# Kernel tuning notes

Measured on AMD Instinct MI355X. Metric: run time of the kernel, lower is better.

The kernel has to match this reference:

```python
import jax, jax.numpy as jnp
import numpy as np

BS, T, D_IN, NH, D_OUT = 8, 1024, 64, 8, 1024
DK = 2


def setup_inputs() -> dict:
    key = jax.random.key(0)
    ks = jax.random.split(key, 10)
    X = jax.random.normal(ks[0], (BS, T, D_IN), dtype=jnp.float32)
    # Linear(d_in, 2*Nh) params (torch stores weight as (out, in))
    Wq_w = jax.random.normal(ks[1], (2 * NH, D_IN), dtype=jnp.float32) * (1.0 / np.sqrt(D_IN))
    Wq_b = jax.random.normal(ks[2], (2 * NH,), dtype=jnp.float32) * 0.02
    Wk_w = jax.random.normal(ks[3], (2 * NH, D_IN), dtype=jnp.float32) * (1.0 / np.sqrt(D_IN))
    Wk_b = jax.random.normal(ks[4], (2 * NH,), dtype=jnp.float32) * 0.02
    Wkey_ = jax.random.normal(ks[5], (2, 2), dtype=jnp.float32)
    u = jax.random.normal(ks[6], (T, 2), dtype=jnp.float32)
    # R[t,l] = [(l-t)^2, (l-t)]
    rel = jnp.arange(T)[None, :] - jnp.arange(T)[:, None]  # (T,T)
    R = jnp.stack([rel.astype(jnp.float32) ** 2, rel.astype(jnp.float32)], axis=-1)  # (T,T,2)
    attention_center = jax.random.normal(ks[7], (NH, 1), dtype=jnp.float32) * 2.0
    alpha = jax.random.normal(ks[8], (1,), dtype=jnp.float32)
    W_w = jax.random.normal(ks[9], (D_OUT, T), dtype=jnp.float32) * (1.0 / np.sqrt(T))
    W_b = jnp.zeros((D_OUT,), dtype=jnp.float32)
    return {"X": X, "Wq_w": Wq_w, "Wq_b": Wq_b, "Wk_w": Wk_w, "Wk_b": Wk_b,
            "Wkey_": Wkey_, "u": u, "R": R, "attention_center": attention_center,
            "alpha": alpha, "W_w": W_w, "W_b": W_b}


def reference(X, Wq_w, Wq_b, Wk_w, Wk_b, Wkey_, u, R, attention_center, alpha, W_w, W_b):
    bs, T_, d_in = X.shape
    Nh = attention_center.shape[0]
    query = (X @ Wq_w.T + Wq_b).reshape(bs, T_, Nh, DK)
    key_ = (X @ Wk_w.T + Wk_b).reshape(bs, T_, Nh, DK)
    r_delta = jnp.einsum('de,tle->tld', Wkey_, R)  # (T,T,2)
    v = -alpha * jnp.concatenate([jnp.ones_like(attention_center), -2.0 * attention_center], axis=-1)  # (Nh,2)
    first = jnp.einsum('bthd,blhd->bthl', query, key_)
    second = jnp.einsum('bthd,tld->bthl', query, r_delta)
    third = jnp.einsum('ld,bthd->blht', u, key_)  # added positionally, matching torch
    fourth = jnp.einsum('hd,tld->thl', v, r_delta)
    scores = first + second + third + fourth[None]  # (bs,T,Nh,T)
    probs = jax.nn.softmax(scores, axis=-1)
    iv = jnp.einsum('bthl,bld->bthd', probs, X)  # (bs,T,Nh,d_in)
    iv = iv.reshape(bs, T_, Nh * d_in).transpose(0, 2, 1)  # (bs, Nh*d_in, T)
    out = iv @ W_w.T + W_b  # (bs, Nh*d_in, d_out)
    return out
```

## Files before the change

### kernel.cpp

```cpp
#include <hip/hip_runtime.h>
#include <hip/hip_bf16.h>

#define BS   8
#define TT   1024
#define DIN  64
#define NH   8
#define DOUT 1024

typedef __attribute__((ext_vector_type(8))) short bf16x8;
typedef __attribute__((ext_vector_type(8))) unsigned short u16x8;
typedef __attribute__((ext_vector_type(4))) float f32x4;

typedef __attribute__((address_space(3))) unsigned int lds_u32;
typedef const __attribute__((address_space(1))) unsigned int glb_u32;

__device__ __forceinline__ unsigned short f2bf(float f) {
    unsigned int u = __float_as_uint(f);
    u += 0x7fff + ((u >> 16) & 1);
    return (unsigned short)(u >> 16);
}

__global__ __launch_bounds__(256) void prep_fused(const float* __restrict__ X,
                                                  const float* __restrict__ Wq_w,
                                                  const float* __restrict__ Wq_b,
                                                  const float* __restrict__ Wk_w,
                                                  const float* __restrict__ Wk_b,
                                                  const float* __restrict__ W_w,
                                                  float* __restrict__ Q,
                                                  float* __restrict__ K,
                                                  unsigned short* __restrict__ XtP,
                                                  unsigned short* __restrict__ Wbf) {
    __shared__ float Ws[32][65];
    __shared__ float bsm[32];
    __shared__ float Xs[8][64];
    __shared__ unsigned short S[64][68];

    const int bid = blockIdx.x, tid = threadIdx.x;

    if (bid < 1024) {
        for (int i = tid; i < 2048; i += 256) {
            int r = i >> 6, d = i & 63;
            Ws[r][d] = (r < 16) ? Wq_w[r * 64 + d] : Wk_w[(r - 16) * 64 + d];
        }
        if (tid < 32) bsm[tid] = (tid < 16) ? Wq_b[tid] : Wk_b[tid - 16];
        int row0 = bid * 8;
        for (int i = tid; i < 512; i += 256) {
            int r = i >> 6, d = i & 63;
            Xs[r][d] = X[(size_t)(row0 + r) * 64 + d];
        }
        __syncthreads();
        int r = tid >> 5;
        int j = tid & 31;
        float s = bsm[j];
        #pragma unroll
        for (int d = 0; d < 64; ++d) s = fmaf(Xs[r][d], Ws[j][d], s);
        int row = row0 + r;
        if (j < 16) {
            Q[(size_t)row * 16 + j] = s;
        } else {
            int h = (j - 16) >> 1, d2 = (j - 16) & 1;
            int b = row >> 10, l = row & 1023;
            K[(((size_t)(b * 8 + h)) * 1024 + l) * 2 + d2] = s;
        }
    } else if (bid < 1152) {
        int idx = bid - 1024;
        int bb = idx >> 4, lc = idx & 15;
        int l0 = lc * 64;
        int r = tid >> 4;
        int q4 = (tid & 15) * 4;
        #pragma unroll
        for (int p = 0; p < 4; ++p) {
            int row = p * 16 + r;
            float4 v = *(const float4*)(X + ((size_t)(bb * 1024 + l0 + row)) * 64 + q4);
            S[row][q4 + 0] = f2bf(v.x);
            S[row][q4 + 1] = f2bf(v.y);
            S[row][q4 + 2] = f2bf(v.z);
            S[row][q4 + 3] = f2bf(v.w);
        }
        __syncthreads();
        #pragma unroll
        for (int it = 0; it < 2; ++it) {
            int chunk = it * 256 + tid;
            int lane = chunk & 63, mi = (chunk >> 6) & 3, lbr = chunk >> 8;
            int g = lane >> 4, tr = lane & 15;
            int d = mi * 16 + tr;
            int ls = lbr * 32 + g * 8;
            u16x8 o;
            #pragma unroll
            for (int j = 0; j < 8; ++j) o[j] = S[ls + j][d];
            *(u16x8*)(XtP + (size_t)((((bb * 32 + lc * 2 + lbr) * 4 + mi) * 64 + lane)) * 8) = o;
        }
    } else {
        int i = (bid - 1152) * 256 + tid;
        float4 v = ((const float4*)W_w)[i];
        ushort4 o;
        o.x = f2bf(v.x); o.y = f2bf(v.y); o.z = f2bf(v.z); o.w = f2bf(v.w);
        ((ushort4*)Wbf)[i] = o;
    }
}

__global__ __launch_bounds__(256, 8) void attn_mfma(const unsigned short* __restrict__ XtP,
                                                    const float* __restrict__ Q,
                                                    const float* __restrict__ K,
                                                    const float* __restrict__ u,
                                                    const float* __restrict__ Wkey,
                                                    const float* __restrict__ center,
                                                    const float* __restrict__ alpha,
                                                    unsigned short* __restrict__ IV) {
    const int h  = blockIdx.y;
    const int bb = blockIdx.z;
    const int tid = threadIdx.x;
    const int w = tid >> 6, lane = tid & 63;
    const int g = lane >> 4, tr = lane & 15;
    const int tsub = w & 1, lhalf = w >> 1;
    const int t = blockIdx.x * 32 + tsub * 16 + tr;

    __shared__ float SH[2176];
    __shared__ float red[4][4];

    {
        const float4* Kg = (const float4*)(K + ((size_t)(bb * 8 + h)) * 2048);
        float4* Ks4 = (float4*)SH;
        Ks4[tid] = Kg[tid];
        Ks4[tid + 256] = Kg[tid + 256];
    }
    __syncthreads();

    float mxp = -1e30f, mxn = 1e30f, myp = -1e30f, myn = 1e30f;
    {
        const float2* K2 = (const float2*)SH;
        #pragma unroll
        for (int i = 0; i < 4; ++i) {
            float2 kk = K2[tid + i * 256];
            mxp = fmaxf(mxp, kk.x); mxn = fminf(mxn, kk.x);
            myp = fmaxf(myp, kk.y); myn = fminf(myn, kk.y);
        }
        #pragma unroll
        for (int off = 32; off; off >>= 1) {
            mxp = fmaxf(mxp, __shfl_xor(mxp, off)); mxn = fminf(mxn, __shfl_xor(mxn, off));
            myp = fmaxf(myp, __shfl_xor(myp, off)); myn = fminf(myn, __shfl_xor(myn, off));
        }
        if (lane == 0) { red[w][0] = mxp; red[w][1] = mxn; red[w][2] = myp; red[w][3] = myn; }
    }
    __syncthreads();
    mxp = fmaxf(fmaxf(red[0][0], red[1][0]), fmaxf(red[2][0], red[3][0]));
    mxn = fminf(fminf(red[0][1], red[1][1]), fminf(red[2][1], red[3][1]));
    myp = fmaxf(fmaxf(red[0][2], red[1][2]), fmaxf(red[2][2], red[3][2]));
    myn = fminf(fminf(red[0][3], red[1][3]), fminf(red[2][3], red[3][3]));

    const float L2E = 1.4426950408889634f;
    float2 q  = ((const float2*)Q)[(size_t)(bb * 1024 + t) * 8 + h];
    float2 uu = ((const float2*)u)[t];
    const float al = alpha[0];
    const float a0 = (q.x + uu.x) * L2E;
    const float a1 = (q.y + uu.y) * L2E;
    const float p0 = q.x - al;
    const float p1 = q.y + 2.0f * al * center[h];
    const float c0 = (p0 * Wkey[0] + p1 * Wkey[2]) * L2E;
    const float c1 = (p0 * Wkey[1] + p1 * Wkey[3]) * L2E;
    const float tf = (float)t;

    const float qb = fmaxf(a0 * mxp, a0 * mxn) + fmaxf(a1 * myp, a1 * myn);
    const float dlo = -tf, dhi = 1023.0f - tf;
    float qm = fmaxf(fmaf(fmaf(c0, dlo, c1), dlo, 0.0f),
                     fmaf(fmaf(c0, dhi, c1), dhi, 0.0f));
    if (c0 < 0.0f) {
        float dstar = -c1 / (2.0f * c0);
        if (dstar > dlo && dstar < dhi) qm = -c1 * c1 / (4.0f * c0);
    }
    const float negm = -(qm + qb);

    f32x4 acc[4];
    #pragma unroll
    for (int mi = 0; mi < 4; ++mi) acc[mi] = (f32x4){0.f, 0.f, 0.f, 0.f};
    float sum = 0.f;

    const bf16x8* XtPv = (const bf16x8*)XtP;
    const size_t xbase = ((size_t)(bb * 32 + lhalf * 16) * 4) * 64 + lane;

    for (int it = 0; it < 16; ++it) {
        const int l0 = lhalf * 512 + it * 32;
        const int lb = l0 + g * 8;
        const float4* kp = (const float4*)SH + (lb >> 1);
        const float dlb = (float)lb - tf;
        union { bf16x8 v; unsigned int wd[4]; } pb;
        #pragma unroll
        for (int jj = 0; jj < 4; ++jj) {
            float4 kv = kp[jj];
            float dl0 = dlb + (float)(2 * jj);
            float dl1 = dl0 + 1.0f;
            float e0 = exp2f(fmaf(fmaf(c0, dl0, c1), dl0, fmaf(a0, kv.x, fmaf(a1, kv.y, negm))));
            float e1 = exp2f(fmaf(fmaf(c0, dl1, c1), dl1, fmaf(a0, kv.z, fmaf(a1, kv.w, negm))));
            sum += e0 + e1;
            asm("v_cvt_pk_bf16_f32 %0, %1, %2" : "=v"(pb.wd[jj]) : "v"(e0), "v"(e1));
        }
        #pragma unroll
        for (int mi = 0; mi < 4; ++mi)
            acc[mi] = __builtin_amdgcn_mfma_f32_16x16x32_bf16(
                XtPv[xbase + (size_t)it * 256 + mi * 64], pb.v, acc[mi], 0, 0, 0);
    }

    sum += __shfl_xor(sum, 16);
    sum += __shfl_xor(sum, 32);

    __syncthreads();
    if (lhalf == 1) {
        float* cp = SH + (tsub * 64 + lane) * 17;
        #pragma unroll
        for (int mi = 0; mi < 4; ++mi)
            #pragma unroll
            for (int r = 0; r < 4; ++r) cp[mi * 4 + r] = acc[mi][r];
        cp[16] = sum;
    }
    __syncthreads();
    if (lhalf == 0) {
        const float* cp = SH + (tsub * 64 + lane) * 17;
        #pragma unroll
        for (int mi = 0; mi < 4; ++mi)
            #pragma unroll
            for (int r = 0; r < 4; ++r) acc[mi][r] += cp[mi * 4 + r];
        sum += cp[16];
        const float rinv = 1.0f / sum;
        #pragma unroll
        for (int mi = 0; mi < 4; ++mi) {
            #pragma unroll
            for (int r = 0; r < 4; ++r) {
                int d = mi * 16 + g * 4 + r;
                IV[((size_t)(bb * 512 + h * 64 + d)) * 1024 + t] = f2bf(acc[mi][r] * rinv);
            }
        }
    }
}

__global__ __launch_bounds__(256) void gemm_out(const unsigned short* __restrict__ IV,
                                                const unsigned short* __restrict__ Wbf,
                                                const float* __restrict__ W_b,
                                                float* __restrict__ out) {
    const int jt = blockIdx.x;
    const int mt = blockIdx.y;
    const int tid = threadIdx.x;
    const int w = tid >> 6, lane = tid & 63;
    const int lr = lane & 15, kg = lane >> 4;
    const int wr = w >> 1, wc = w & 1;

    __shared__ unsigned short As[2][128 * 32];
    __shared__ unsigned short Bs[2][128 * 32];

    const int r0 = tid >> 2, s0 = tid & 3;
    const int kg0 = s0 ^ ((r0 >> 1) & 3);
    const int kg1 = s0 ^ (((r0 + 64) >> 1) & 3);
    const unsigned short* Ag0 = IV  + (size_t)(mt * 128 + r0) * 1024 + kg0 * 8;
    const unsigned short* Ag1 = IV  + (size_t)(mt * 128 + r0 + 64) * 1024 + kg1 * 8;
    const unsigned short* Bg0 = Wbf + (size_t)(jt * 128 + r0) * 1024 + kg0 * 8;
    const unsigned short* Bg1 = Wbf + (size_t)(jt * 128 + r0 + 64) * 1024 + kg1 * 8;

#define STAGE(bufi, kk) do {                                                                   \
    __builtin_amdgcn_global_load_lds((glb_u32*)(Ag0 + (kk)), (lds_u32*)(&As[bufi][tid * 8]), 16, 0, 0);          \
    __builtin_amdgcn_global_load_lds((glb_u32*)(Ag1 + (kk)), (lds_u32*)(&As[bufi][(tid + 256) * 8]), 16, 0, 0);  \
    __builtin_amdgcn_global_load_lds((glb_u32*)(Bg0 + (kk)), (lds_u32*)(&Bs[bufi][tid * 8]), 16, 0, 0);          \
    __builtin_amdgcn_global_load_lds((glb_u32*)(Bg1 + (kk)), (lds_u32*)(&Bs[bufi][(tid + 256) * 8]), 16, 0, 0);  \
} while (0)

    f32x4 acc[4][4];
    #pragma unroll
    for (int mi = 0; mi < 4; ++mi)
        #pragma unroll
        for (int ni = 0; ni < 4; ++ni)
            acc[mi][ni] = (f32x4){0.f, 0.f, 0.f, 0.f};

    STAGE(0, 0);
    asm volatile("s_waitcnt vmcnt(0)");
    __syncthreads();

    const int slot = kg ^ ((lr >> 1) & 3);
    int cur = 0;
    for (int kt = 0; kt < 32; ++kt) {
        if (kt < 31) STAGE(cur ^ 1, (kt + 1) * 32);
        bf16x8 af[4], bfr[4];
        #pragma unroll
        for (int mi = 0; mi < 4; ++mi) {
            int row = wr * 64 + mi * 16 + lr;
            af[mi] = *(const bf16x8*)(&As[cur][row * 32 + slot * 8]);
        }
        #pragma unroll
        for (int ni = 0; ni < 4; ++ni) {
            int row = wc * 64 + ni * 16 + lr;
            bfr[ni] = *(const bf16x8*)(&Bs[cur][row * 32 + slot * 8]);
        }
        #pragma unroll
        for (int mi = 0; mi < 4; ++mi)
            #pragma unroll
            for (int ni = 0; ni < 4; ++ni)
                acc[mi][ni] = __builtin_amdgcn_mfma_f32_16x16x32_bf16(
                    af[mi], bfr[ni], acc[mi][ni], 0, 0, 0);
        asm volatile("s_waitcnt vmcnt(0)");
        __syncthreads();
        cur ^= 1;
    }
#undef STAGE

    float wb[4];
    #pragma unroll
    for (int ni = 0; ni < 4; ++ni) wb[ni] = W_b[jt * 128 + wc * 64 + ni * 16 + lr];

    #pragma unroll
    for (int mi = 0; mi < 4; ++mi) {
        #pragma unroll
        for (int ni = 0; ni < 4; ++ni) {
            #pragma unroll
            for (int r = 0; r < 4; ++r) {
                int m = mt * 128 + wr * 64 + mi * 16 + kg * 4 + r;
                int j = jt * 128 + wc * 64 + ni * 16 + lr;
                out[(size_t)m * 1024 + j] = acc[mi][ni][r] + wb[ni];
            }
        }
    }
}

extern "C" void kernel_launch(void* const* d_in, const int* in_sizes, int n_in,
                              void* d_out, int out_size, void* d_ws, size_t ws_size,
                              hipStream_t stream) {
    const float* X      = (const float*)d_in[0];
    const float* Wq_w   = (const float*)d_in[1];
    const float* Wq_b   = (const float*)d_in[2];
    const float* Wk_w   = (const float*)d_in[3];
    const float* Wk_b   = (const float*)d_in[4];
    const float* Wkey   = (const float*)d_in[5];
    const float* u      = (const float*)d_in[6];
    const float* center = (const float*)d_in[8];
    const float* alpha  = (const float*)d_in[9];
    const float* W_w    = (const float*)d_in[10];
    const float* W_b    = (const float*)d_in[11];
    float* out = (float*)d_out;

    char* ws = (char*)d_ws;
    unsigned short* XtP  = (unsigned short*)ws;
    float*          Qbuf = (float*)(ws + (1024u << 10));
    float*          Kbuf = (float*)(ws + (1536u << 10));
    unsigned short* Wbf  = (unsigned short*)(ws + (2048u << 10));
    unsigned short* IV   = (unsigned short*)(ws + (4096u << 10));

    prep_fused<<<2176, 256, 0, stream>>>(X, Wq_w, Wq_b, Wk_w, Wk_b, W_w, Qbuf, Kbuf, XtP, Wbf);
    attn_mfma<<<dim3(32, 8, 8), 256, 0, stream>>>(XtP, Qbuf, Kbuf, u, Wkey, center, alpha, IV);
    gemm_out<<<dim3(8, 32), 256, 0, stream>>>(IV, Wbf, W_b, out);
}
```

Baseline: 151.7 us.

## Stage X tiles in LDS with double buffering and use 512-thread blocks

The attention kernel now uses 512-thread blocks covering 64 query rows. Each X tile is loaded once into a double-buffered LDS buffer with async global-to-LDS loads and shared by all wavefronts, instead of every wave reading XtP from global memory. The output GEMM also moves to 512 threads with an 8-wave 2x4 layout and half the accumulators per wave. This cuts redundant global traffic and register pressure, but adds a block-wide barrier every iteration and may lower occupancy.

After: 144.6 us. 4.7% less time.

```diff
diff --git a/kernel.cpp b/kernel.cpp
--- a/kernel.cpp
+++ b/kernel.cpp
@@ -99,7 +99,7 @@
     }
 }
 
-__global__ __launch_bounds__(256, 8) void attn_mfma(const unsigned short* __restrict__ XtP,
+__global__ __launch_bounds__(512, 8) void attn_mfma(const unsigned short* __restrict__ XtP,
                                                     const float* __restrict__ Q,
                                                     const float* __restrict__ K,
                                                     const float* __restrict__ u,
@@ -112,29 +112,30 @@
     const int tid = threadIdx.x;
     const int w = tid >> 6, lane = tid & 63;
     const int g = lane >> 4, tr = lane & 15;
-    const int tsub = w & 1, lhalf = w >> 1;
-    const int t = blockIdx.x * 32 + tsub * 16 + tr;
-
-    __shared__ float SH[2176];
-    __shared__ float red[4][4];
+    const int tsub = w & 3, lhalf = w >> 2;
+    const int t = blockIdx.x * 64 + tsub * 16 + tr;
+
+    __shared__ float SH[4352];
+    __shared__ unsigned short Xs[2][4096];
+    __shared__ float red[8][4];
+
+    const unsigned short* xsrc = XtP + (size_t)bb * 65536
+                               + (size_t)((tid >> 8) * 16) * 2048 + (tid & 255) * 8;
 
     {
         const float4* Kg = (const float4*)(K + ((size_t)(bb * 8 + h)) * 2048);
-        float4* Ks4 = (float4*)SH;
-        Ks4[tid] = Kg[tid];
-        Ks4[tid + 256] = Kg[tid + 256];
-    }
-    __syncthreads();
-
-    float mxp = -1e30f, mxn = 1e30f, myp = -1e30f, myn = 1e30f;
+        ((float4*)SH)[tid] = Kg[tid];
+        __builtin_amdgcn_global_load_lds((glb_u32*)xsrc, (lds_u32*)(&Xs[0][tid * 8]), 16, 0, 0);
+    }
+    asm volatile("s_waitcnt vmcnt(0)");
+    __syncthreads();
+
+    float mxp, mxn, myp, myn;
     {
         const float2* K2 = (const float2*)SH;
-        #pragma unroll
-        for (int i = 0; i < 4; ++i) {
-            float2 kk = K2[tid + i * 256];
-            mxp = fmaxf(mxp, kk.x); mxn = fminf(mxn, kk.x);
-            myp = fmaxf(myp, kk.y); myn = fminf(myn, kk.y);
-        }
+        float2 ka = K2[tid], kb = K2[tid + 512];
+        mxp = fmaxf(ka.x, kb.x); mxn = fminf(ka.x, kb.x);
+        myp = fmaxf(ka.y, kb.y); myn = fminf(ka.y, kb.y);
         #pragma unroll
         for (int off = 32; off; off >>= 1) {
             mxp = fmaxf(mxp, __shfl_xor(mxp, off)); mxn = fminf(mxn, __shfl_xor(mxn, off));
@@ -143,10 +144,12 @@
         if (lane == 0) { red[w][0] = mxp; red[w][1] = mxn; red[w][2] = myp; red[w][3] = myn; }
     }
     __syncthreads();
-    mxp = fmaxf(fmaxf(red[0][0], red[1][0]), fmaxf(red[2][0], red[3][0]));
-    mxn = fminf(fminf(red[0][1], red[1][1]), fminf(red[2][1], red[3][1]));
-    myp = fmaxf(fmaxf(red[0][2], red[1][2]), fmaxf(red[2][2], red[3][2]));
-    myn = fminf(fminf(red[0][3], red[1][3]), fminf(red[2][3], red[3][3]));
+    mxp = red[0][0]; mxn = red[0][1]; myp = red[0][2]; myn = red[0][3];
+    #pragma unroll
+    for (int i = 1; i < 8; ++i) {
+        mxp = fmaxf(mxp, red[i][0]); mxn = fminf(mxn, red[i][1]);
+        myp = fmaxf(myp, red[i][2]); myn = fminf(myn, red[i][3]);
+    }
 
     const float L2E = 1.4426950408889634f;
     float2 q  = ((const float2*)Q)[(size_t)(bb * 1024 + t) * 8 + h];
@@ -175,12 +178,13 @@
     for (int mi = 0; mi < 4; ++mi) acc[mi] = (f32x4){0.f, 0.f, 0.f, 0.f};
     float sum = 0.f;
 
-    const bf16x8* XtPv = (const bf16x8*)XtP;
-    const size_t xbase = ((size_t)(bb * 32 + lhalf * 16) * 4) * 64 + lane;
-
+    int cur = 0;
     for (int it = 0; it < 16; ++it) {
-        const int l0 = lhalf * 512 + it * 32;
-        const int lb = l0 + g * 8;
+        const int itn = (it + 1) & 15;
+        __builtin_amdgcn_global_load_lds((glb_u32*)(xsrc + itn * 2048),
+                                         (lds_u32*)(&Xs[cur ^ 1][tid * 8]), 16, 0, 0);
+
+        const int lb = lhalf * 512 + it * 32 + g * 8;
         const float4* kp = (const float4*)SH + (lb >> 1);
         const float dlb = (float)lb - tf;
         union { bf16x8 v; unsigned int wd[4]; } pb;
@@ -194,10 +198,15 @@
             sum += e0 + e1;
             asm("v_cvt_pk_bf16_f32 %0, %1, %2" : "=v"(pb.wd[jj]) : "v"(e0), "v"(e1));
         }
+        const bf16x8* xv = (const bf16x8*)(&Xs[cur][0]);
         #pragma unroll
         for (int mi = 0; mi < 4; ++mi)
             acc[mi] = __builtin_amdgcn_mfma_f32_16x16x32_bf16(
-                XtPv[xbase + (size_t)it * 256 + mi * 64], pb.v, acc[mi], 0, 0, 0);
+                xv[lhalf * 256 + mi * 64 + lane], pb.v, acc[mi], 0, 0, 0);
+
+        asm volatile("s_waitcnt vmcnt(0)");
+        __syncthreads();
+        cur ^= 1;
     }
 
     sum += __shfl_xor(sum, 16);
@@ -232,7 +241,7 @@
     }
 }
 
-__global__ __launch_bounds__(256) void gemm_out(const unsigned short* __restrict__ IV,
+__global__ __launch_bounds__(512) void gemm_out(const unsigned short* __restrict__ IV,
                                                 const unsigned short* __restrict__ Wbf,
                                                 const float* __restrict__ W_b,
                                                 float* __restrict__ out) {
@@ -241,31 +250,26 @@
     const int tid = threadIdx.x;
     const int w = tid >> 6, lane = tid & 63;
     const int lr = lane & 15, kg = lane >> 4;
-    const int wr = w >> 1, wc = w & 1;
-
-    __shared__ unsigned short As[2][128 * 32];
-    __shared__ unsigned short Bs[2][128 * 32];
+    const int wr = w >> 2, wc = w & 3;
+
+    __shared__ unsigned short As[2][4096];
+    __shared__ unsigned short Bs[2][4096];
 
     const int r0 = tid >> 2, s0 = tid & 3;
-    const int kg0 = s0 ^ ((r0 >> 1) & 3);
-    const int kg1 = s0 ^ (((r0 + 64) >> 1) & 3);
-    const unsigned short* Ag0 = IV  + (size_t)(mt * 128 + r0) * 1024 + kg0 * 8;
-    const unsigned short* Ag1 = IV  + (size_t)(mt * 128 + r0 + 64) * 1024 + kg1 * 8;
-    const unsigned short* Bg0 = Wbf + (size_t)(jt * 128 + r0) * 1024 + kg0 * 8;
-    const unsigned short* Bg1 = Wbf + (size_t)(jt * 128 + r0 + 64) * 1024 + kg1 * 8;
-
-#define STAGE(bufi, kk) do {                                                                   \
-    __builtin_amdgcn_global_load_lds((glb_u32*)(Ag0 + (kk)), (lds_u32*)(&As[bufi][tid * 8]), 16, 0, 0);          \
-    __builtin_amdgcn_global_load_lds((glb_u32*)(Ag1 + (kk)), (lds_u32*)(&As[bufi][(tid + 256) * 8]), 16, 0, 0);  \
-    __builtin_amdgcn_global_load_lds((glb_u32*)(Bg0 + (kk)), (lds_u32*)(&Bs[bufi][tid * 8]), 16, 0, 0);          \
-    __builtin_amdgcn_global_load_lds((glb_u32*)(Bg1 + (kk)), (lds_u32*)(&Bs[bufi][(tid + 256) * 8]), 16, 0, 0);  \
+    const int kgA = s0 ^ ((r0 >> 1) & 3);
+    const unsigned short* Ag = IV  + (size_t)(mt * 128 + r0) * 1024 + kgA * 8;
+    const unsigned short* Bg = Wbf + (size_t)(jt * 128 + r0) * 1024 + kgA * 8;
+
+#define STAGE(bufi, kk) do {                                                                          \
+    __builtin_amdgcn_global_load_lds((glb_u32*)(Ag + (kk)), (lds_u32*)(&As[bufi][tid * 8]), 16, 0, 0); \
+    __builtin_amdgcn_global_load_lds((glb_u32*)(Bg + (kk)), (lds_u32*)(&Bs[bufi][tid * 8]), 16, 0, 0); \
 } while (0)
 
-    f32x4 acc[4][4];
+    f32x4 acc[4][2];
     #pragma unroll
     for (int mi = 0; mi < 4; ++mi)
         #pragma unroll
-        for (int ni = 0; ni < 4; ++ni)
+        for (int ni = 0; ni < 2; ++ni)
             acc[mi][ni] = (f32x4){0.f, 0.f, 0.f, 0.f};
 
     STAGE(0, 0);
@@ -276,21 +280,21 @@
     int cur = 0;
     for (int kt = 0; kt < 32; ++kt) {
         if (kt < 31) STAGE(cur ^ 1, (kt + 1) * 32);
-        bf16x8 af[4], bfr[4];
+        bf16x8 af[4], bfr[2];
         #pragma unroll
         for (int mi = 0; mi < 4; ++mi) {
             int row = wr * 64 + mi * 16 + lr;
             af[mi] = *(const bf16x8*)(&As[cur][row * 32 + slot * 8]);
         }
         #pragma unroll
-        for (int ni = 0; ni < 4; ++ni) {
-            int row = wc * 64 + ni * 16 + lr;
+        for (int ni = 0; ni < 2; ++ni) {
+            int row = wc * 32 + ni * 16 + lr;
             bfr[ni] = *(const bf16x8*)(&Bs[cur][row * 32 + slot * 8]);
         }
         #pragma unroll
         for (int mi = 0; mi < 4; ++mi)
             #pragma unroll
-            for (int ni = 0; ni < 4; ++ni)
+            for (int ni = 0; ni < 2; ++ni)
                 acc[mi][ni] = __builtin_amdgcn_mfma_f32_16x16x32_bf16(
                     af[mi], bfr[ni], acc[mi][ni], 0, 0, 0);
         asm volatile("s_waitcnt vmcnt(0)");
@@ -299,18 +303,18 @@
     }
 #undef STAGE
 
-    float wb[4];
-    #pragma unroll
-    for (int ni = 0; ni < 4; ++ni) wb[ni] = W_b[jt * 128 + wc * 64 + ni * 16 + lr];
+    float wb[2];
+    #pragma unroll
+    for (int ni = 0; ni < 2; ++ni) wb[ni] = W_b[jt * 128 + wc * 32 + ni * 16 + lr];
 
     #pragma unroll
     for (int mi = 0; mi < 4; ++mi) {
         #pragma unroll
-        for (int ni = 0; ni < 4; ++ni) {
+        for (int ni = 0; ni < 2; ++ni) {
             #pragma unroll
             for (int r = 0; r < 4; ++r) {
                 int m = mt * 128 + wr * 64 + mi * 16 + kg * 4 + r;
-                int j = jt * 128 + wc * 64 + ni * 16 + lr;
+                int j = jt * 128 + wc * 32 + ni * 16 + lr;
                 out[(size_t)m * 1024 + j] = acc[mi][ni][r] + wb[ni];
             }
         }
@@ -341,6 +345,6 @@
     unsigned short* IV   = (unsigned short*)(ws + (4096u << 10));
 
     prep_fused<<<2176, 256, 0, stream>>>(X, Wq_w, Wq_b, Wk_w, Wk_b, W_w, Qbuf, Kbuf, XtP, Wbf);
-    attn_mfma<<<dim3(32, 8, 8), 256, 0, stream>>>(XtP, Qbuf, Kbuf, u, Wkey, center, alpha, IV);
-    gemm_out<<<dim3(8, 32), 256, 0, stream>>>(IV, Wbf, W_b, out);
-}
+    attn_mfma<<<dim3(16, 8, 8), 512, 0, stream>>>(XtP, Qbuf, Kbuf, u, Wkey, center, alpha, IV);
+    gemm_out<<<dim3(8, 32), 512, 0, stream>>>(IV, Wbf, W_b, out);
+}
```
